# Kernel tuning notes

Hardware: AMD Instinct MI355X
Metric: run time of the kernel (lower is better)

The kernel has to match this reference:

```python
import jax, jax.numpy as jnp
import numpy as np

N_NODES = 100000


def _gcn_layer(x, W, b, src, dst, dinv):
    # x: [N, din]; W: [din, dout]; src/dst: [E+N] (self-loops included); dinv: [N]
    h = x @ W                                   # [N, dout] small GEMM
    norm = dinv[src] * dinv[dst]                # [E+N]
    msg = h[src] * norm[:, None]                # [E+N, dout] gather
    out = jax.ops.segment_sum(msg, dst, num_segments=N_NODES)  # scatter-add
    return jax.nn.relu(out + b)


def setup_inputs() -> dict:
    key = jax.random.key(0)
    ks = jax.random.split(key, 8)
    d_in, d_h = 128, 128
    x = jax.random.normal(ks[0], (N_NODES, d_in), dtype=jnp.float32)
    edge_index = jax.random.randint(ks[1], (2, 1600000), 0, N_NODES, dtype=jnp.int64)
    def glorot(k, din, dout):
        lim = np.sqrt(6.0 / (din + dout)).astype(np.float32)
        return jax.random.uniform(k, (din, dout), jnp.float32, -lim, lim)
    W1 = glorot(ks[2], d_in, d_h); b1 = jnp.zeros((d_h,), jnp.float32)
    W2 = glorot(ks[3], d_h, d_h); b2 = jnp.zeros((d_h,), jnp.float32)
    W3 = glorot(ks[4], d_h, d_h); b3 = jnp.zeros((d_h,), jnp.float32)
    return {"x": x, "W1": W1, "b1": b1, "W2": W2, "b2": b2,
            "W3": W3, "b3": b3, "edge_index": edge_index}


def reference(x, W1, b1, W2, b2, W3, b3, edge_index):
    # GCNConv (Kipf & Welling): D^{-1/2}(A+I)D^{-1/2} X W + b, per layer, with ReLU.
    loop = jnp.arange(N_NODES, dtype=edge_index.dtype)
    src = jnp.concatenate([edge_index[0], loop])  # self-loops appended
    dst = jnp.concatenate([edge_index[1], loop])
    deg = jax.ops.segment_sum(jnp.ones_like(dst, dtype=x.dtype), dst,
                              num_segments=N_NODES)
    dinv = jnp.where(deg > 0, jax.lax.rsqrt(deg), 0.0)
    h = _gcn_layer(x, W1, b1, src, dst, dinv)
    h = _gcn_layer(h, W2, b2, src, dst, dinv)
    h = _gcn_layer(h, W3, b3, src, dst, dinv)
    return h
```

## Files before the change

### kernel.cpp

```cpp
#include <hip/hip_runtime.h>
#include <hip/hip_fp16.h>
#include <math.h>

#define NN 100000
#define DD 128
#define AGG_BLOCKS 2048

#define NBUCK 98
#define BSH 10
#define BW 1024
#define CAP 18432
#define APASS 196
#define CURPAD 32

typedef short short8 __attribute__((ext_vector_type(8)));
typedef _Float16 half8 __attribute__((ext_vector_type(8)));
typedef float f32x4 __attribute__((ext_vector_type(4)));

__global__ __launch_bounds__(256) void bucket_scatter_kernel(
    const int* __restrict__ src, const int* __restrict__ dst, int E,
    int* __restrict__ cur, int* __restrict__ packed)
{
    __shared__ int h[NBUCK];
    __shared__ int base[NBUCK];
    __shared__ int c2[NBUCK];

    const int tid = threadIdx.x;
    const int chunk = (E + APASS - 1) / APASS;
    const int e0 = blockIdx.x * chunk;
    const int e1 = min(e0 + chunk, E);

    if (tid < NBUCK) { h[tid] = 0; c2[tid] = 0; }
    __syncthreads();

    for (int e = e0 + tid; e < e1; e += 256)
        atomicAdd(&h[dst[e] >> BSH], 1);
    __syncthreads();

    if (tid < NBUCK && h[tid] > 0)
        base[tid] = atomicAdd(&cur[tid * CURPAD], h[tid]);
    __syncthreads();

    for (int e = e0 + tid; e < e1; e += 256) {
        int d = dst[e];
        int b = d >> BSH;
        int r = atomicAdd(&c2[b], 1);
        int pos = base[b] + r;
        if (pos < CAP)
            packed[b * CAP + pos] = ((d & (BW - 1)) << 17) | src[e];
    }
}

__global__ void bucket_scan_kernel(const int* __restrict__ cur,
                                   int* __restrict__ cbase,
                                   int* __restrict__ offsets) {
    if (threadIdx.x == 0) {
        int run = 0;
        for (int b = 0; b < NBUCK; ++b) {
            int c = cur[b * CURPAD];
            if (c > CAP) c = CAP;
            cbase[b] = run;
            run += c;
        }
        offsets[NN] = run;
    }
}

__global__ __launch_bounds__(256) void bucket_csr_kernel(
    const int* __restrict__ cur, const int* __restrict__ cbase,
    const int* __restrict__ packed,
    int* __restrict__ offsets, float* __restrict__ dinv,
    int* __restrict__ csr)
{
    __shared__ int cnt[BW];
    __shared__ int excl[BW];
    __shared__ int ts[256];

    const int tid = threadIdx.x;
    const int b = blockIdx.x;
    int c = cur[b * CURPAD];
    if (c > CAP) c = CAP;
    const int cb = cbase[b];
    const int pbase = b * CAP;

    #pragma unroll
    for (int k = 0; k < 4; ++k) cnt[tid * 4 + k] = 0;
    __syncthreads();

    for (int i = tid; i < c; i += 256)
        atomicAdd(&cnt[packed[pbase + i] >> 17], 1);
    __syncthreads();

    int v[4];
    int s = 0;
    #pragma unroll
    for (int k = 0; k < 4; ++k) { v[k] = cnt[tid * 4 + k]; s += v[k]; }
    ts[tid] = s;
    __syncthreads();
    for (int d = 1; d < 256; d <<= 1) {
        int t = (tid >= d) ? ts[tid - d] : 0;
        __syncthreads();
        ts[tid] += t;
        __syncthreads();
    }
    int ex = ts[tid] - s;

    int run = 0;
    #pragma unroll
    for (int k = 0; k < 4; ++k) {
        int dl = tid * 4 + k;
        excl[dl] = ex + run;
        int node = b * BW + dl;
        if (node < NN) {
            offsets[node] = cb + ex + run;
            dinv[node] = rsqrtf((float)v[k] + 1.0f);
        }
        run += v[k];
    }
    __syncthreads();

    for (int i = tid; i < c; i += 256) {
        int p = packed[pbase + i];
        int dl = p >> 17;
        int r = atomicAdd(&excl[dl], 1);
        csr[cb + r] = p & 0x1FFFF;
    }
}

__device__ __forceinline__ unsigned short f2bf(float f) {
    unsigned int u = __float_as_uint(f);
    unsigned int r = u + 0x7FFFu + ((u >> 16) & 1u);
    return (unsigned short)(r >> 16);
}

__device__ __forceinline__ void split8(const float* v, short8& hi, short8& lo) {
    #pragma unroll
    for (int j = 0; j < 8; ++j) {
        float f = v[j];
        unsigned short h = f2bf(f);
        float fl = f - __uint_as_float(((unsigned int)h) << 16);
        hi[j] = (short)h;
        lo[j] = (short)f2bf(fl);
    }
}

__device__ __forceinline__ void split8h(const float* v, half8& hi, half8& lo) {
    #pragma unroll
    for (int j = 0; j < 8; ++j) {
        _Float16 h = (_Float16)v[j];
        float fl = v[j] - (float)h;
        hi[j] = h;
        lo[j] = (_Float16)fl;
    }
}

__device__ __forceinline__ void split8t(const float* v, short8& hi, short8& lo) {
    const unsigned int* u = (const unsigned int*)v;
    float lof[8];
    #pragma unroll
    for (int j = 0; j < 8; ++j)
        lof[j] = v[j] - __uint_as_float(u[j] & 0xFFFF0000u);
    const unsigned int* lu = (const unsigned int*)lof;
    union { short8 s; unsigned int w[4]; } H, L;
    #pragma unroll
    for (int q = 0; q < 4; ++q) {
#if __has_builtin(__builtin_amdgcn_perm)
        H.w[q] = __builtin_amdgcn_perm(u[2 * q + 1], u[2 * q], 0x07060302u);
        L.w[q] = __builtin_amdgcn_perm(lu[2 * q + 1], lu[2 * q], 0x07060302u);
#else
        H.w[q] = (u[2 * q + 1] & 0xFFFF0000u) | (u[2 * q] >> 16);
        L.w[q] = (lu[2 * q + 1] & 0xFFFF0000u) | (lu[2 * q] >> 16);
#endif
    }
    hi = H.s; lo = L.s;
}

__global__ __launch_bounds__(256) void wsplit3_kernel(const float* __restrict__ W1,
                                                      const float* __restrict__ W2,
                                                      const float* __restrict__ W3,
                                                      uint4* __restrict__ wh,
                                                      uint4* __restrict__ wl) {
    int b = blockIdx.x;
    int layer = b >> 3;
    const float* W = (layer == 0) ? W1 : (layer == 1) ? W2 : W3;
    int i = (b & 7) * 256 + threadIdx.x;
    int lane_e = i & 63;
    int ks = (i >> 6) & 3;
    int cf = i >> 8;
    int colb = cf * 16 + (lane_e & 15);
    int rowb = ks * 32 + (lane_e >> 4) * 8;
    float wvv[8];
    #pragma unroll
    for (int j = 0; j < 8; ++j) wvv[j] = W[(rowb + j) * DD + colb];
    if (layer == 0) {
        short8 h, l;
        split8(wvv, h, l);
        union { short8 s; uint4 u; } ch, cl;
        ch.s = h; cl.s = l;
        wh[i] = ch.u;
        wl[i] = cl.u;
    } else {
        half8 h, l;
        split8h(wvv, h, l);
        union { half8 s; uint4 u; } ch, cl;
        ch.s = h; cl.s = l;
        wh[layer * 2048 + i] = ch.u;
        wl[layer * 2048 + i] = cl.u;
    }
}

__global__ __launch_bounds__(256) void gemm_norm_kernel(
    const float* __restrict__ X, const uint4* __restrict__ whg,
    const uint4* __restrict__ wlg,
    const float* __restrict__ dinv, __half* __restrict__ G)
{
    const int tid  = threadIdx.x;
    const int base = blockIdx.x * 128;
    const int lane = tid & 63;
    const int wv   = tid >> 6;
    const int kg   = lane >> 4;
    const int mcol = lane & 15;

    const int node0 = base + wv * 32 + mcol;
    const int node1 = node0 + 16;

    short8 xh[2][4], xl[2][4];
    #pragma unroll
    for (int rf = 0; rf < 2; ++rf) {
        int arow = rf ? node1 : node0;
        if (arow >= NN) arow = NN - 1;
        const float* xr = X + (size_t)arow * DD;
        #pragma unroll
        for (int ks = 0; ks < 4; ++ks) {
            int k0 = ks * 32 + kg * 8;
            float av[8];
            *(float4*)&av[0] = *(const float4*)&xr[k0];
            *(float4*)&av[4] = *(const float4*)&xr[k0 + 4];
            split8t(av, xh[rf][ks], xl[rf][ks]);
        }
    }
    const float di0 = dinv[node0 < NN ? node0 : NN - 1];
    const float di1 = dinv[node1 < NN ? node1 : NN - 1];

    uint4 bh[4], bl[4], bhn[4], bln[4];
    #pragma unroll
    for (int ks = 0; ks < 4; ++ks) {
        bh[ks] = whg[ks * 64 + lane];
        bl[ks] = wlg[ks * 64 + lane];
    }

    #pragma unroll 1
    for (int cf = 0; cf < 8; ++cf) {
        if (cf < 7) {
            #pragma unroll
            for (int ks = 0; ks < 4; ++ks) {
                bhn[ks] = whg[((cf + 1) * 4 + ks) * 64 + lane];
                bln[ks] = wlg[((cf + 1) * 4 + ks) * 64 + lane];
            }
        }
        f32x4 acc0 = {0.f, 0.f, 0.f, 0.f};
        f32x4 acc1 = {0.f, 0.f, 0.f, 0.f};
        #pragma unroll
        for (int ks = 0; ks < 4; ++ks) {
            union { uint4 u; short8 s; } ch, cl;
            ch.u = bh[ks];
            cl.u = bl[ks];
            acc0 = __builtin_amdgcn_mfma_f32_16x16x32_bf16(ch.s, xh[0][ks], acc0, 0, 0, 0);
            acc0 = __builtin_amdgcn_mfma_f32_16x16x32_bf16(cl.s, xh[0][ks], acc0, 0, 0, 0);
            acc0 = __builtin_amdgcn_mfma_f32_16x16x32_bf16(ch.s, xl[0][ks], acc0, 0, 0, 0);
            acc1 = __builtin_amdgcn_mfma_f32_16x16x32_bf16(ch.s, xh[1][ks], acc1, 0, 0, 0);
            acc1 = __builtin_amdgcn_mfma_f32_16x16x32_bf16(cl.s, xh[1][ks], acc1, 0, 0, 0);
            acc1 = __builtin_amdgcn_mfma_f32_16x16x32_bf16(ch.s, xl[1][ks], acc1, 0, 0, 0);
        }
        const int fb = cf * 16 + kg * 4;
        if (node0 < NN) {
            __half2 p0 = __floats2half2_rn(acc0[0] * di0, acc0[1] * di0);
            __half2 p1 = __floats2half2_rn(acc0[2] * di0, acc0[3] * di0);
            uint2 st;
            st.x = *reinterpret_cast<unsigned int*>(&p0);
            st.y = *reinterpret_cast<unsigned int*>(&p1);
            *(uint2*)&G[(size_t)node0 * DD + fb] = st;
        }
        if (node1 < NN) {
            __half2 p0 = __floats2half2_rn(acc1[0] * di1, acc1[1] * di1);
            __half2 p1 = __floats2half2_rn(acc1[2] * di1, acc1[3] * di1);
            uint2 st;
            st.x = *reinterpret_cast<unsigned int*>(&p0);
            st.y = *reinterpret_cast<unsigned int*>(&p1);
            *(uint2*)&G[(size_t)node1 * DD + fb] = st;
        }
        #pragma unroll
        for (int ks = 0; ks < 4; ++ks) { bh[ks] = bhn[ks]; bl[ks] = bln[ks]; }
    }
}

__global__ __launch_bounds__(256) void gemm_f16_kernel(
    const __half* __restrict__ X, const uint4* __restrict__ whg,
    const uint4* __restrict__ wlg,
    const float* __restrict__ dinv, __half* __restrict__ G)
{
    const int tid  = threadIdx.x;
    const int base = blockIdx.x * 128;
    const int lane = tid & 63;
    const int wv   = tid >> 6;
    const int kg   = lane >> 4;
    const int mcol = lane & 15;

    const int node0 = base + wv * 32 + mcol;
    const int node1 = node0 + 16;

    uint4 xb[2][4];
    #pragma unroll
    for (int rf = 0; rf < 2; ++rf) {
        int arow = rf ? node1 : node0;
        if (arow >= NN) arow = NN - 1;
        const __half* xr = X + (size_t)arow * DD;
        #pragma unroll
        for (int ks = 0; ks < 4; ++ks)
            xb[rf][ks] = *(const uint4*)&xr[ks * 32 + kg * 8];
    }
    const float di0 = dinv[node0 < NN ? node0 : NN - 1];
    const float di1 = dinv[node1 < NN ? node1 : NN - 1];

    uint4 ah[4], al[4], ahn[4], aln[4];
    #pragma unroll
    for (int ks = 0; ks < 4; ++ks) {
        ah[ks] = whg[ks * 64 + lane];
        al[ks] = wlg[ks * 64 + lane];
    }

    #pragma unroll 1
    for (int cf = 0; cf < 8; ++cf) {
        if (cf < 7) {
            #pragma unroll
            for (int ks = 0; ks < 4; ++ks) {
                ahn[ks] = whg[((cf + 1) * 4 + ks) * 64 + lane];
                aln[ks] = wlg[((cf + 1) * 4 + ks) * 64 + lane];
            }
        }
        f32x4 acc0 = {0.f, 0.f, 0.f, 0.f};
        f32x4 acc1 = {0.f, 0.f, 0.f, 0.f};
        #pragma unroll
        for (int ks = 0; ks < 4; ++ks) {
            union { uint4 u; half8 h; } wh_, wl_, x0, x1;
            wh_.u = ah[ks]; wl_.u = al[ks];
            x0.u = xb[0][ks]; x1.u = xb[1][ks];
            acc0 = __builtin_amdgcn_mfma_f32_16x16x32_f16(wh_.h, x0.h, acc0, 0, 0, 0);
            acc0 = __builtin_amdgcn_mfma_f32_16x16x32_f16(wl_.h, x0.h, acc0, 0, 0, 0);
            acc1 = __builtin_amdgcn_mfma_f32_16x16x32_f16(wh_.h, x1.h, acc1, 0, 0, 0);
            acc1 = __builtin_amdgcn_mfma_f32_16x16x32_f16(wl_.h, x1.h, acc1, 0, 0, 0);
        }
        const int fb = cf * 16 + kg * 4;
        if (node0 < NN) {
            __half2 p0 = __floats2half2_rn(acc0[0] * di0, acc0[1] * di0);
            __half2 p1 = __floats2half2_rn(acc0[2] * di0, acc0[3] * di0);
            uint2 st;
            st.x = *reinterpret_cast<unsigned int*>(&p0);
            st.y = *reinterpret_cast<unsigned int*>(&p1);
            *(uint2*)&G[(size_t)node0 * DD + fb] = st;
        }
        if (node1 < NN) {
            __half2 p0 = __floats2half2_rn(acc1[0] * di1, acc1[1] * di1);
            __half2 p1 = __floats2half2_rn(acc1[2] * di1, acc1[3] * di1);
            uint2 st;
            st.x = *reinterpret_cast<unsigned int*>(&p0);
            st.y = *reinterpret_cast<unsigned int*>(&p1);
            *(uint2*)&G[(size_t)node1 * DD + fb] = st;
        }
        #pragma unroll
        for (int ks = 0; ks < 4; ++ks) { ah[ks] = ahn[ks]; al[ks] = aln[ks]; }
    }
}

__device__ __forceinline__ float4 gload(const __half* __restrict__ g, int idx, int cq) {
    uint2 u = *(const uint2*)(g + (size_t)idx * DD + cq * 4);
    __half2 h0 = *reinterpret_cast<const __half2*>(&u.x);
    __half2 h1 = *reinterpret_cast<const __half2*>(&u.y);
    float2 f0 = __half22float2(h0);
    float2 f1 = __half22float2(h1);
    return make_float4(f0.x, f0.y, f1.x, f1.y);
}

__device__ __forceinline__ float4 gather_row(const __half* __restrict__ g,
                                             const int* __restrict__ off,
                                             const int* __restrict__ csr,
                                             const float* __restrict__ dinv,
                                             const float4 bb, int node,
                                             int sub, int cq) {
    float4 acc = make_float4(0.f, 0.f, 0.f, 0.f);
    float4 acc2 = make_float4(0.f, 0.f, 0.f, 0.f);
    if (sub == 0) acc = gload(g, node, cq);

    const int e0 = off[node], end = off[node + 1];
    const int cnt = end - e0;
    const int pairs = cnt >> 1;
    const int np4 = pairs & ~3;

    if (np4) {
        int i0 = csr[e0 + 0 + sub];
        int i1 = csr[e0 + 2 + sub];
        int i2 = csr[e0 + 4 + sub];
        int i3 = csr[e0 + 6 + sub];
        for (int p = 4; p < np4; p += 4) {
            int b0 = e0 + 2 * p + sub;
            int j0 = csr[b0];
            int j1 = csr[b0 + 2];
            int j2 = csr[b0 + 4];
            int j3 = csr[b0 + 6];
            float4 v0 = gload(g, i0, cq);
            float4 v1 = gload(g, i1, cq);
            float4 v2 = gload(g, i2, cq);
            float4 v3 = gload(g, i3, cq);
            acc.x += v0.x + v2.x; acc.y += v0.y + v2.y;
            acc.z += v0.z + v2.z; acc.w += v0.w + v2.w;
            acc2.x += v1.x + v3.x; acc2.y += v1.y + v3.y;
            acc2.z += v1.z + v3.z; acc2.w += v1.w + v3.w;
            i0 = j0; i1 = j1; i2 = j2; i3 = j3;
        }
        float4 v0 = gload(g, i0, cq);
        float4 v1 = gload(g, i1, cq);
        float4 v2 = gload(g, i2, cq);
        float4 v3 = gload(g, i3, cq);
        acc.x += v0.x + v2.x; acc.y += v0.y + v2.y;
        acc.z += v0.z + v2.z; acc.w += v0.w + v2.w;
        acc2.x += v1.x + v3.x; acc2.y += v1.y + v3.y;
        acc2.z += v1.z + v3.z; acc2.w += v1.w + v3.w;
    }
    for (int q = np4; q < pairs; ++q) {
        int s = csr[e0 + 2 * q + sub];
        float4 v = gload(g, s, cq);
        acc.x += v.x; acc.y += v.y; acc.z += v.z; acc.w += v.w;
    }
    if ((cnt & 1) && sub == 0) {
        int s = csr[end - 1];
        float4 v = gload(g, s, cq);
        acc.x += v.x; acc.y += v.y; acc.z += v.z; acc.w += v.w;
    }

    acc.x += acc2.x; acc.y += acc2.y; acc.z += acc2.z; acc.w += acc2.w;
    acc.x += __shfl_xor(acc.x, 32, 64);
    acc.y += __shfl_xor(acc.y, 32, 64);
    acc.z += __shfl_xor(acc.z, 32, 64);
    acc.w += __shfl_xor(acc.w, 32, 64);

    float di = dinv[node];
    float4 o;
    o.x = fmaxf(fmaf(acc.x, di, bb.x), 0.f);
    o.y = fmaxf(fmaf(acc.y, di, bb.y), 0.f);
    o.z = fmaxf(fmaf(acc.z, di, bb.z), 0.f);
    o.w = fmaxf(fmaf(acc.w, di, bb.w), 0.f);
    return o;
}

template <typename OutT>
__global__ __launch_bounds__(256) void agg_kernel(
    const __half* __restrict__ g, const float* __restrict__ dinv,
    const int* __restrict__ off, const int* __restrict__ csr,
    const float* __restrict__ bias, OutT* __restrict__ out)
{
    const int wid  = threadIdx.x >> 6;
    const int lane = threadIdx.x & 63;
    const int sub  = lane >> 5;
    const int cq   = lane & 31;
    const float4 bb = ((const float4*)bias)[cq];
    const int ngroups = (NN + 3) / 4;

    for (int grp = blockIdx.x; grp < ngroups; grp += AGG_BLOCKS) {
        int node = grp * 4 + wid;
        if (node >= NN) continue;
        float4 o = gather_row(g, off, csr, dinv, bb, node, sub, cq);
        if (sub == 0) {
            if constexpr (sizeof(OutT) == 4) {
                ((float4*)out)[(size_t)node * 32 + cq] = o;
            } else {
                uint2 st;
                __half2 h0 = __floats2half2_rn(o.x, o.y);
                __half2 h1 = __floats2half2_rn(o.z, o.w);
                st.x = *reinterpret_cast<unsigned int*>(&h0);
                st.y = *reinterpret_cast<unsigned int*>(&h1);
                *(uint2*)((__half*)out + (size_t)node * DD + cq * 4) = st;
            }
        }
    }
}

extern "C" void kernel_launch(void* const* d_in, const int* in_sizes, int n_in,
                              void* d_out, int out_size, void* d_ws, size_t ws_size,
                              hipStream_t stream)
{
    const float* x  = (const float*)d_in[0];
    const float* W1 = (const float*)d_in[1];
    const float* b1 = (const float*)d_in[2];
    const float* W2 = (const float*)d_in[3];
    const float* b2 = (const float*)d_in[4];
    const float* W3 = (const float*)d_in[5];
    const float* b3 = (const float*)d_in[6];
    const int*   ei = (const int*)d_in[7];

    const int E = in_sizes[7] / 2;
    const int* src = ei;
    const int* dst = ei + E;

    float* out = (float*)d_out;

    char* wsb = (char*)d_ws;
    size_t p = 0;
    int* offsets  = (int*)(wsb + p); p += ((size_t)(NN + 1) * 4 + 1023) & ~1023ull;
    int* csr      = (int*)(wsb + p); p += ((size_t)E * 4 + 1023) & ~1023ull;
    float* dinv   = (float*)(wsb + p); p += ((size_t)NN * 4 + 1023) & ~1023ull;
    int* cur      = (int*)(wsb + p); p += (size_t)NBUCK * CURPAD * 4;
    int* cbase    = (int*)(wsb + p); p += 1024;
    uint4* wh     = (uint4*)(wsb + p); p += 3 * 2048 * sizeof(uint4);
    uint4* wl     = (uint4*)(wsb + p); p += 3 * 2048 * sizeof(uint4);
    int* packed   = (int*)(wsb + p); p += ((size_t)NBUCK * CAP * 4 + 1023) & ~1023ull;
    __half* g     = (__half*)(wsb + p); p += (size_t)NN * DD * 2;
    __half* g2    = (__half*)(wsb + p); p += (size_t)NN * DD * 2;

    hipMemsetAsync(cur, 0, (size_t)NBUCK * CURPAD * 4, stream);
    bucket_scatter_kernel<<<APASS, 256, 0, stream>>>(src, dst, E, cur, packed);
    bucket_scan_kernel<<<1, 64, 0, stream>>>(cur, cbase, offsets);
    bucket_csr_kernel<<<NBUCK, 256, 0, stream>>>(cur, cbase, packed, offsets, dinv, csr);
    wsplit3_kernel<<<24, 256, 0, stream>>>(W1, W2, W3, wh, wl);

    const int gemm_grid = (NN + 127) / 128;

    gemm_norm_kernel<<<gemm_grid, 256, 0, stream>>>(x, wh, wl, dinv, g);
    agg_kernel<__half><<<AGG_BLOCKS, 256, 0, stream>>>(g, dinv, offsets, csr, b1, g2);
    gemm_f16_kernel<<<gemm_grid, 256, 0, stream>>>(g2, wh + 2048, wl + 2048, dinv, g);
    agg_kernel<__half><<<AGG_BLOCKS, 256, 0, stream>>>(g, dinv, offsets, csr, b2, g2);
    gemm_f16_kernel<<<gemm_grid, 256, 0, stream>>>(g2, wh + 4096, wl + 4096, dinv, g);
    agg_kernel<float><<<AGG_BLOCKS, 256, 0, stream>>>(g, dinv, offsets, csr, b3, out);
}
```

Measured before the change: 358.6 us.

## Halve bucket width and split CSR build into count and fill kernels

Doubles the number of dst buckets (512 nodes each) and the scatter grid, folds the single-thread bucket scan into each count block's own prefix scan, and splits CSR construction into a per-bucket count kernel and a four-way split fill kernel that uses global per-node atomic cursors. The goal is more parallelism in the graph preprocessing and removal of the serial scan launch. The cost is global atomics instead of shared ones in the fill step, plus an extra cursor array.

```diff
diff --git a/kernel.cpp b/kernel.cpp
--- a/kernel.cpp
+++ b/kernel.cpp
@@ -6,11 +6,12 @@
 #define DD 128
 #define AGG_BLOCKS 2048
 
-#define NBUCK 98
-#define BSH 10
-#define BW 1024
-#define CAP 18432
-#define APASS 196
+#define NBUCK 196
+#define BSH 9
+#define BW 512
+#define CAP 10240
+#define APASS 392
+#define FILLB (NBUCK * 4)
 #define CURPAD 32
 
 typedef short short8 __attribute__((ext_vector_type(8)));
@@ -51,51 +52,34 @@
     }
 }
 
-__global__ void bucket_scan_kernel(const int* __restrict__ cur,
-                                   int* __restrict__ cbase,
-                                   int* __restrict__ offsets) {
-    if (threadIdx.x == 0) {
-        int run = 0;
-        for (int b = 0; b < NBUCK; ++b) {
-            int c = cur[b * CURPAD];
-            if (c > CAP) c = CAP;
-            cbase[b] = run;
-            run += c;
-        }
-        offsets[NN] = run;
-    }
-}
-
-__global__ __launch_bounds__(256) void bucket_csr_kernel(
-    const int* __restrict__ cur, const int* __restrict__ cbase,
-    const int* __restrict__ packed,
-    int* __restrict__ offsets, float* __restrict__ dinv,
-    int* __restrict__ csr)
+__global__ __launch_bounds__(256) void bucket_count_kernel(
+    const int* __restrict__ cur, const int* __restrict__ packed,
+    int* __restrict__ offsets, int* __restrict__ cursor,
+    float* __restrict__ dinv)
 {
     __shared__ int cnt[BW];
-    __shared__ int excl[BW];
     __shared__ int ts[256];
+    __shared__ int cbase_sh;
 
     const int tid = threadIdx.x;
     const int b = blockIdx.x;
+
+    cnt[tid] = 0;
+    cnt[tid + 256] = 0;
+    __syncthreads();
+
     int c = cur[b * CURPAD];
     if (c > CAP) c = CAP;
-    const int cb = cbase[b];
     const int pbase = b * CAP;
-
-    #pragma unroll
-    for (int k = 0; k < 4; ++k) cnt[tid * 4 + k] = 0;
-    __syncthreads();
-
     for (int i = tid; i < c; i += 256)
         atomicAdd(&cnt[packed[pbase + i] >> 17], 1);
-    __syncthreads();
-
-    int v[4];
-    int s = 0;
-    #pragma unroll
-    for (int k = 0; k < 4; ++k) { v[k] = cnt[tid * 4 + k]; s += v[k]; }
-    ts[tid] = s;
+
+    int myc = 0;
+    if (tid < NBUCK) {
+        myc = cur[tid * CURPAD];
+        if (myc > CAP) myc = CAP;
+    }
+    ts[tid] = myc;
     __syncthreads();
     for (int d = 1; d < 256; d <<= 1) {
         int t = (tid >= d) ? ts[tid - d] : 0;
@@ -103,27 +87,61 @@
         ts[tid] += t;
         __syncthreads();
     }
+    if (tid == 0) cbase_sh = (b > 0) ? ts[b - 1] : 0;
+    if (b == 0 && tid == 0) offsets[NN] = ts[NBUCK - 1];
+    __syncthreads();
+    const int cb = cbase_sh;
+
+    int v0 = cnt[tid * 2];
+    int v1 = cnt[tid * 2 + 1];
+    int s = v0 + v1;
+    __syncthreads();
+    ts[tid] = s;
+    __syncthreads();
+    for (int d = 1; d < 256; d <<= 1) {
+        int t = (tid >= d) ? ts[tid - d] : 0;
+        __syncthreads();
+        ts[tid] += t;
+        __syncthreads();
+    }
     int ex = ts[tid] - s;
 
-    int run = 0;
-    #pragma unroll
-    for (int k = 0; k < 4; ++k) {
-        int dl = tid * 4 + k;
-        excl[dl] = ex + run;
-        int node = b * BW + dl;
-        if (node < NN) {
-            offsets[node] = cb + ex + run;
-            dinv[node] = rsqrtf((float)v[k] + 1.0f);
-        }
-        run += v[k];
-    }
-    __syncthreads();
-
-    for (int i = tid; i < c; i += 256) {
+    int node0 = (b << BSH) + tid * 2;
+    if (node0 < NN) {
+        int o0 = cb + ex;
+        offsets[node0] = o0;
+        cursor[node0] = o0;
+        dinv[node0] = rsqrtf((float)v0 + 1.0f);
+    }
+    int node1 = node0 + 1;
+    if (node1 < NN) {
+        int o1 = cb + ex + v0;
+        offsets[node1] = o1;
+        cursor[node1] = o1;
+        dinv[node1] = rsqrtf((float)v1 + 1.0f);
+    }
+}
+
+__global__ __launch_bounds__(256) void bucket_fill_kernel(
+    const int* __restrict__ cur, const int* __restrict__ packed,
+    int* __restrict__ cursor, int* __restrict__ csr)
+{
+    const int tid = threadIdx.x;
+    const int b = blockIdx.x >> 2;
+    const int q = blockIdx.x & 3;
+
+    int c = cur[b * CURPAD];
+    if (c > CAP) c = CAP;
+    const int qs = (c + 3) >> 2;
+    const int i0 = q * qs;
+    const int i1 = min(i0 + qs, c);
+    const int pbase = b * CAP;
+
+    for (int i = i0 + tid; i < i1; i += 256) {
         int p = packed[pbase + i];
-        int dl = p >> 17;
-        int r = atomicAdd(&excl[dl], 1);
-        csr[cb + r] = p & 0x1FFFF;
+        int node = (b << BSH) + (p >> 17);
+        int pos = atomicAdd(&cursor[node], 1);
+        csr[pos] = p & 0x1FFFF;
     }
 }
 
@@ -508,8 +526,8 @@
     int* offsets  = (int*)(wsb + p); p += ((size_t)(NN + 1) * 4 + 1023) & ~1023ull;
     int* csr      = (int*)(wsb + p); p += ((size_t)E * 4 + 1023) & ~1023ull;
     float* dinv   = (float*)(wsb + p); p += ((size_t)NN * 4 + 1023) & ~1023ull;
+    int* cursor   = (int*)(wsb + p); p += ((size_t)NN * 4 + 1023) & ~1023ull;
     int* cur      = (int*)(wsb + p); p += (size_t)NBUCK * CURPAD * 4;
-    int* cbase    = (int*)(wsb + p); p += 1024;
     uint4* wh     = (uint4*)(wsb + p); p += 3 * 2048 * sizeof(uint4);
     uint4* wl     = (uint4*)(wsb + p); p += 3 * 2048 * sizeof(uint4);
     int* packed   = (int*)(wsb + p); p += ((size_t)NBUCK * CAP * 4 + 1023) & ~1023ull;
@@ -518,8 +536,8 @@
 
     hipMemsetAsync(cur, 0, (size_t)NBUCK * CURPAD * 4, stream);
     bucket_scatter_kernel<<<APASS, 256, 0, stream>>>(src, dst, E, cur, packed);
-    bucket_scan_kernel<<<1, 64, 0, stream>>>(cur, cbase, offsets);
-    bucket_csr_kernel<<<NBUCK, 256, 0, stream>>>(cur, cbase, packed, offsets, dinv, csr);
+    bucket_count_kernel<<<NBUCK, 256, 0, stream>>>(cur, packed, offsets, cursor, dinv);
+    bucket_fill_kernel<<<FILLB, 256, 0, stream>>>(cur, packed, cursor, csr);
     wsplit3_kernel<<<24, 256, 0, stream>>>(W1, W2, W3, wh, wl);
 
     const int gemm_grid = (NN + 127) / 128;
```

New measurement: 366.6 us. 1.02x slower.
